# Optimization experiments

Measured on AMD Instinct MI355X. Metric: run time of the kernel, lower is better.

Reference implementation:

```python
import jax, jax.numpy as jnp
import numpy as np

B, N, C, Cn, M = 4, 8192, 128, 64, 32


def _window(x, M):
    # torch F.pad(x, [0,0, M//2, M//2-1]) + unfold(dim=1, size=M, step=1)
    # x: [B, N, Cn] -> [B, N, M, Cn]
    Bx, Nx, Cx = x.shape
    p = M // 2
    xp = jnp.pad(x, ((0, 0), (p, M - 1 - p), (0, 0)))
    idx = jnp.arange(Nx)[:, None] + jnp.arange(M)[None, :]  # [N, M]
    return xp[:, idx, :]  # [B, N, M, Cn]


def setup_inputs() -> dict:
    key = jax.random.key(0)
    ks = jax.random.split(key, 9)
    q = jax.random.normal(ks[0], (B, N, C), dtype=jnp.float32)
    k = jax.random.normal(ks[1], (B, N, C), dtype=jnp.float32)
    v = jax.random.normal(ks[2], (B, N, C), dtype=jnp.float32)
    pe = jax.random.normal(ks[3], (B, N, M, Cn), dtype=jnp.float32)
    # Linear weights stored as [in, out]; scaled like torch default init (~1/sqrt(fan_in)).
    Wq = jax.random.normal(ks[4], (C, Cn), dtype=jnp.float32) / np.sqrt(C)
    Wk = jax.random.normal(ks[5], (C, Cn), dtype=jnp.float32) / np.sqrt(C)
    Wv = jax.random.normal(ks[6], (C, Cn), dtype=jnp.float32) / np.sqrt(C)
    w_sa1 = jax.random.normal(ks[7], (Cn,), dtype=jnp.float32) / np.sqrt(Cn)
    w_sa2 = jax.random.normal(ks[8], (Cn, C), dtype=jnp.float32) / np.sqrt(Cn)
    return {"q": q, "k": k, "v": v, "pe": pe, "Wq": Wq, "Wk": Wk, "Wv": Wv,
            "w_sa1": w_sa1, "w_sa2": w_sa2}


def reference(q, k, v, pe, Wq, Wk, Wv, w_sa1, w_sa2):
    Mw = pe.shape[2]
    qp = q @ Wq  # [B, N, Cn]
    kp = k @ Wk
    vp = v @ Wv
    k_m = _window(kp, Mw)  # [B, N, M, Cn]
    v_m = _window(vp, Mw)  # [B, N, M, Cn]
    # subtraction-based scoring + tiny linear to scalar
    sa = qp[:, :, None, :] - k_m + pe               # [B, N, M, Cn]
    logits = jnp.einsum('bnmc,c->bnm', sa, w_sa1)    # [B, N, M]
    scores = jax.nn.softmax(logits, axis=-1)         # [B, N, M]
    # original: matmul(scores[B,1,N,M], (v_m+pe).permute(0,3,2,1)[B,Cn,M,N]) -> [B,Cn,N,N], sum over last axis.
    # Equivalent: reduce (v_m + pe) over the position axis first, then contract over M.
    S = jnp.sum(v_m + pe, axis=1)                    # [B, M, Cn]
    p_attn = jnp.einsum('bnm,bmc->bnc', scores, S)   # [B, N, Cn]
    out = p_attn @ w_sa2                             # [B, N, C]
    return out  # dropout is identity at eval
```

## Files before the change

kernel.cpp:

```cpp
#include <hip/hip_runtime.h>
#include <math.h>

#define B_ 4
#define N_ 8192
#define C_ 128
#define CN_ 64
#define M_ 32

#define ROR1 0x121
#define ROR2 0x122
#define ROR4 0x124
#define ROR8 0x128

typedef float f4 __attribute__((ext_vector_type(4)));
typedef float f2 __attribute__((ext_vector_type(2)));

__device__ __forceinline__ f4 ld4(const float* p) { return *(const f4*)p; }

template<int CTRL>
__device__ __forceinline__ float dpp_add(float x) {
    int y = __builtin_amdgcn_update_dpp(0, __float_as_int(x), CTRL, 0xF, 0xF, true);
    return x + __int_as_float(y);
}
template<int CTRL>
__device__ __forceinline__ float dpp_max(float x) {
    int y = __builtin_amdgcn_update_dpp(0, __float_as_int(x), CTRL, 0xF, 0xF, true);
    return fmaxf(x, __int_as_float(y));
}
__device__ __forceinline__ float red16_add(float x) {
    return dpp_add<ROR1>(dpp_add<ROR2>(dpp_add<ROR4>(dpp_add<ROR8>(x))));
}
__device__ __forceinline__ float red16_max(float x) {
    return dpp_max<ROR1>(dpp_max<ROR2>(dpp_max<ROR4>(dpp_max<ROR8>(x))));
}

__global__ __launch_bounds__(256) void kA(const float* __restrict__ q,
                                          const float* __restrict__ k,
                                          const float* __restrict__ v,
                                          const float* __restrict__ pe,
                                          const float* __restrict__ Wq,
                                          const float* __restrict__ Wk,
                                          const float* __restrict__ w1,
                                          float* __restrict__ vsum_part,
                                          float* __restrict__ scl_g,
                                          float* __restrict__ pe_part) {
    __shared__ float lpd[4][256];
    __shared__ __align__(16) f4 lps4[4][256];
    __shared__ float pro[352];

    int g = blockIdx.x;
    int t = threadIdx.x;
    int lane = t & 63, wv = t >> 6;

    if (g < 1024) {
        int b = g >> 8;
        int n0 = (g & 255) * 32;
        int grp = lane >> 4, li = lane & 15;
        float* wq1l = pro;
        float* wk1l = pro + 128;
        float* aL   = pro + 256;
        float* kbL  = pro + 288;

        if (t < C_) {
            float s = 0.f;
            for (int c2 = 0; c2 < CN_; ++c2) s += Wq[t * CN_ + c2] * w1[c2];
            wq1l[t] = s;
        } else {
            int c = t - C_;
            float s = 0.f;
            for (int c2 = 0; c2 < CN_; ++c2) s += Wk[c * CN_ + c2] * w1[c2];
            wk1l[c] = s;
        }
        __syncthreads();

        {
            f4 wk0 = *((const f4*)wk1l + li * 2);
            f4 wk1v = *((const f4*)wk1l + li * 2 + 1);
#pragma unroll
            for (int it = 0; it < 4; ++it) {
                int rl = wv * 16 + it * 4 + grp;
                int jrow = n0 - 16 + rl;
                float tk = 0.f;
                if (jrow >= 0 && jrow < N_) {
                    const float* kr = k + ((size_t)b * N_ + jrow) * C_;
                    f4 y0 = ld4(kr + li * 8), y1 = ld4(kr + li * 8 + 4);
                    tk = y0.x * wk0.x + y0.y * wk0.y + y0.z * wk0.z + y0.w * wk0.w
                       + y1.x * wk1v.x + y1.y * wk1v.y + y1.z * wk1v.z + y1.w * wk1v.w;
                }
                tk = red16_add(tk);
                if (li == 0) kbL[rl] = tk;
            }
            f4 wq0 = *((const f4*)wq1l + li * 2);
            f4 wq1v = *((const f4*)wq1l + li * 2 + 1);
#pragma unroll
            for (int it = 0; it < 2; ++it) {
                int rl = wv * 8 + it * 4 + grp;
                const float* qr = q + ((size_t)b * N_ + n0 + rl) * C_;
                f4 x0 = ld4(qr + li * 8), x1 = ld4(qr + li * 8 + 4);
                float ta = x0.x * wq0.x + x0.y * wq0.y + x0.z * wq0.z + x0.w * wq0.w
                         + x1.x * wq1v.x + x1.y * wq1v.y + x1.z * wq1v.z + x1.w * wq1v.w;
                ta = red16_add(ta);
                if (li == 0) aL[rl] = ta;
            }
        }
        __syncthreads();

        f4 w1v = *((const f4*)w1 + li);
        f4 acc[8];
#pragma unroll
        for (int j = 0; j < 8; ++j) acc[j] = (f4){0.f, 0.f, 0.f, 0.f};

        int nbase = n0 + wv * 8;
        const float* pbase = pe + ((size_t)b * N_ + (size_t)nbase) * 2048;
        for (int i = 0; i < 8; ++i) {
            const float* p = pbase + (size_t)i * 2048;
            f4 x[8];
#pragma unroll
            for (int j = 0; j < 8; ++j) x[j] = ld4(p + (j * 64 + lane) * 4);
#pragma unroll
            for (int j = 0; j < 8; ++j) {
                acc[j] += x[j];
                float tv = x[j].x * w1v.x + x[j].y * w1v.y + x[j].z * w1v.z + x[j].w * w1v.w;
                tv = red16_add(tv);
                if (li == 0) lpd[wv][i * 32 + j * 4 + grp] = tv;
            }
        }

        {
            int hw = lane >> 5, m = lane & 31;
            float* sout = scl_g + ((size_t)b * N_ + (size_t)nbase) * M_;
#pragma unroll
            for (int ii = 0; ii < 4; ++ii) {
                int rl = ii * 2 + hw;
                int rb = wv * 8 + rl;
                float pd = lpd[wv][rl * 32 + m];
                float lg = aL[rb] + pd - kbL[rb + m];
                float mx = red16_max(lg);
                mx = fmaxf(mx, __shfl_xor(mx, 16));
                float e = __expf(lg - mx);
                float sm = red16_add(e);
                sm += __shfl_xor(sm, 16);
                sout[ii * 64 + lane] = e / sm;
            }
        }

        f4* ppg = (f4*)(pe_part + (size_t)g * 2048);
#pragma unroll
        for (int r = 0; r < 2; ++r) {
            __syncthreads();
#pragma unroll
            for (int jr = 0; jr < 4; ++jr) lps4[wv][jr * 64 + lane] = acc[r * 4 + jr];
            __syncthreads();
            f4 s = lps4[0][t];
            s += lps4[1][t];
            s += lps4[2][t];
            s += lps4[3][t];
            ppg[r * 256 + t] = s;
        }
    } else {
        int gg = g - 1024;
        int b = gg >> 6;
        int chunk = gg & 63;
        const float* vb = v + ((size_t)b * N_ + (size_t)chunk * 128) * C_;
        int c4 = t & 31, h = t >> 5;
        f4 acc = (f4){0.f, 0.f, 0.f, 0.f};
        for (int r = h; r < 128; r += 8) acc += ld4(vb + (size_t)r * C_ + c4 * 4);
        f4* red = &lps4[0][0];
        red[t] = acc;
        __syncthreads();
        if (t < 32) {
            f4 s = red[t];
#pragma unroll
            for (int i = 1; i < 8; ++i) s += red[i * 32 + t];
            *((f4*)(vsum_part + (size_t)gg * C_) + t) = s;
        }
    }
}

__global__ __launch_bounds__(256) void kR(const float* __restrict__ pe_part,
                                          const float* __restrict__ vsum_part,
                                          float* __restrict__ S_sum,
                                          float* __restrict__ vsum_final) {
    int g = blockIdx.x;
    int t = threadIdx.x;
    if (g < 256) {
        int b = g >> 6, ch = g & 63;
        int pg = t >> 5, fi = t & 31;
        const float* base = pe_part + (size_t)b * 256 * 2048 + ch * 32 + fi;
        float a0 = 0.f, a1 = 0.f, a2 = 0.f, a3 = 0.f;
#pragma unroll
        for (int p = pg; p < 256; p += 32) {
            a0 += base[(size_t)p * 2048];
            a1 += base[(size_t)(p + 8) * 2048];
            a2 += base[(size_t)(p + 16) * 2048];
            a3 += base[(size_t)(p + 24) * 2048];
        }
        __shared__ float red[8][32];
        red[pg][fi] = (a0 + a1) + (a2 + a3);
        __syncthreads();
        if (t < 32) {
            float s = red[0][t];
#pragma unroll
            for (int i = 1; i < 8; ++i) s += red[i][t];
            S_sum[(size_t)b * 2048 + ch * 32 + t] = s;
        }
    } else {
        int b = g - 256;
        if (t < C_) {
            const float* vp = vsum_part + (size_t)b * 64 * C_ + t;
            float a0 = 0.f, a1 = 0.f, a2 = 0.f, a3 = 0.f;
#pragma unroll
            for (int i = 0; i < 64; i += 4) {
                a0 += vp[(i + 0) * C_];
                a1 += vp[(i + 1) * C_];
                a2 += vp[(i + 2) * C_];
                a3 += vp[(i + 3) * C_];
            }
            vsum_final[b * C_ + t] = (a0 + a1) + (a2 + a3);
        }
    }
}

__global__ __launch_bounds__(256) void kB2(const float* __restrict__ v,
                                           const float* __restrict__ Wv,
                                           const float* __restrict__ vsum_final,
                                           const float* __restrict__ S_sum,
                                           const float* __restrict__ w2,
                                           float* __restrict__ SW2) {
    int b = blockIdx.x >> 3, seg = blockIdx.x & 7;
    int t = threadIdx.x;
    __shared__ float vd[4][C_];
    __shared__ float Sl[4][CN_];
#pragma unroll
    for (int mlp = 0; mlp < 2; ++mlp) {
        int ml = (t >> 7) + mlp * 2;
        int c = t & 127;
        int m = seg * 4 + ml;
        float excl = 0.f;
        if (m > 16) {
            for (int r = 0; r < m - 16; ++r) excl += v[((size_t)b * N_ + r) * C_ + c];
        } else if (m < 16) {
            for (int r = N_ - (16 - m); r < N_; ++r) excl += v[((size_t)b * N_ + r) * C_ + c];
        }
        vd[ml][c] = vsum_final[b * C_ + c] - excl;
    }
    __syncthreads();
    {
        int ml = t >> 6, c2 = t & 63;
        float s = 0.f;
        for (int c = 0; c < C_; ++c) s += vd[ml][c] * Wv[c * CN_ + c2];
        s += S_sum[(size_t)b * 2048 + (seg * 4 + ml) * CN_ + c2];
        Sl[ml][c2] = s;
    }
    __syncthreads();
#pragma unroll
    for (int pass = 0; pass < 2; ++pass) {
        int ml = (t >> 7) + pass * 2;
        int cc = t & 127;
        float s = 0.f;
#pragma unroll
        for (int c2 = 0; c2 < CN_; ++c2) s += Sl[ml][c2] * w2[c2 * C_ + cc];
        SW2[((size_t)b * M_ + seg * 4 + ml) * C_ + cc] = s;
    }
}

__global__ __launch_bounds__(256) void kOut2(const float* __restrict__ scl_g,
                                             const float* __restrict__ SW2,
                                             float* __restrict__ out) {
    int g = blockIdx.x;
    int b = g >> 7;
    int n0 = (g & 127) * 64;
    int t = threadIdx.x;
    int lane = t & 63, wv = t >> 6;
    __shared__ float scl[64][M_];

    {
        const f4* src = (const f4*)(scl_g + ((size_t)b * N_ + (size_t)n0) * M_);
        f4* dst = (f4*)&scl[0][0];
        dst[t] = src[t];
        dst[256 + t] = src[256 + t];
    }
    f2 sw2[M_];
    {
        const f2* sw2g = (const f2*)(SW2 + (size_t)b * M_ * C_);
#pragma unroll
        for (int mm = 0; mm < M_; ++mm) sw2[mm] = sw2g[mm * 64 + lane];
    }
    __syncthreads();
    for (int i = 0; i < 16; ++i) {
        int r = wv * 16 + i;
        const f4* sp = (const f4*)(&scl[r][0]);
        float ox = 0.f, oy = 0.f;
#pragma unroll
        for (int j4 = 0; j4 < 8; ++j4) {
            f4 s4 = sp[j4];
            ox += s4.x * sw2[j4 * 4 + 0].x; oy += s4.x * sw2[j4 * 4 + 0].y;
            ox += s4.y * sw2[j4 * 4 + 1].x; oy += s4.y * sw2[j4 * 4 + 1].y;
            ox += s4.z * sw2[j4 * 4 + 2].x; oy += s4.z * sw2[j4 * 4 + 2].y;
            ox += s4.w * sw2[j4 * 4 + 3].x; oy += s4.w * sw2[j4 * 4 + 3].y;
        }
        size_t u = (size_t)b * N_ + (size_t)(n0 + r);
        f2 o; o.x = ox; o.y = oy;
        *((f2*)(out + u * C_) + lane) = o;
    }
}

extern "C" void kernel_launch(void* const* d_in, const int* in_sizes, int n_in,
                              void* d_out, int out_size, void* d_ws, size_t ws_size,
                              hipStream_t stream) {
    const float* q  = (const float*)d_in[0];
    const float* k  = (const float*)d_in[1];
    const float* v  = (const float*)d_in[2];
    const float* pe = (const float*)d_in[3];
    const float* Wq = (const float*)d_in[4];
    const float* Wk = (const float*)d_in[5];
    const float* Wv = (const float*)d_in[6];
    const float* w1 = (const float*)d_in[7];
    const float* w2 = (const float*)d_in[8];
    float* out = (float*)d_out;
    float* ws  = (float*)d_ws;

    float* vsum_part  = ws;
    float* vsum_final = vsum_part + 32768;
    float* scl_g      = vsum_final + 512;
    float* pe_part    = scl_g + 1048576;
    float* S_sum      = pe_part + 2097152;
    float* SW2        = S_sum + 8192;

    kA   <<<1280, 256, 0, stream>>>(q, k, v, pe, Wq, Wk, w1, vsum_part, scl_g, pe_part);
    kR   <<<260, 256, 0, stream>>>(pe_part, vsum_part, S_sum, vsum_final);
    kB2  <<<32, 256, 0, stream>>>(v, Wv, vsum_final, S_sum, w2, SW2);
    kOut2<<<512, 256, 0, stream>>>(scl_g, SW2, out);
}
```

Before: 99.86 us.

## Fold v column-sum blocks into pe blocks and interleave k/q/v loads with pe stream

Removes the separate 256 v-reduction blocks from kA. Each of the 1024 pe blocks now also sums its 32 rows of v, and the k/q projection-dot loads move inside the fully unrolled pe loop so they overlap with the pe streaming. The v partial buffer grows to 256 partials per batch, which kR reduces. Launch bounds now request 4 blocks per SIMD-level occupancy. The risks are higher register pressure from full unrolling and a longer per-block critical path.

```diff
diff --git a/kernel.cpp b/kernel.cpp
--- a/kernel.cpp
+++ b/kernel.cpp
@@ -34,16 +34,20 @@
     return dpp_max<ROR1>(dpp_max<ROR2>(dpp_max<ROR4>(dpp_max<ROR8>(x))));
 }
 
-__global__ __launch_bounds__(256) void kA(const float* __restrict__ q,
-                                          const float* __restrict__ k,
-                                          const float* __restrict__ v,
-                                          const float* __restrict__ pe,
-                                          const float* __restrict__ Wq,
-                                          const float* __restrict__ Wk,
-                                          const float* __restrict__ w1,
-                                          float* __restrict__ vsum_part,
-                                          float* __restrict__ scl_g,
-                                          float* __restrict__ pe_part) {
+__device__ __forceinline__ float dot4(f4 a, f4 b) {
+    return a.x * b.x + a.y * b.y + a.z * b.z + a.w * b.w;
+}
+
+__global__ __launch_bounds__(256, 4) void kA(const float* __restrict__ q,
+                                             const float* __restrict__ k,
+                                             const float* __restrict__ v,
+                                             const float* __restrict__ pe,
+                                             const float* __restrict__ Wq,
+                                             const float* __restrict__ Wk,
+                                             const float* __restrict__ w1,
+                                             float* __restrict__ vsum_part,
+                                             float* __restrict__ scl_g,
+                                             float* __restrict__ pe_part) {
     __shared__ float lpd[4][256];
     __shared__ __align__(16) f4 lps4[4][256];
     __shared__ float pro[352];
@@ -51,129 +55,132 @@
     int g = blockIdx.x;
     int t = threadIdx.x;
     int lane = t & 63, wv = t >> 6;
-
-    if (g < 1024) {
-        int b = g >> 8;
-        int n0 = (g & 255) * 32;
-        int grp = lane >> 4, li = lane & 15;
-        float* wq1l = pro;
-        float* wk1l = pro + 128;
-        float* aL   = pro + 256;
-        float* kbL  = pro + 288;
-
-        if (t < C_) {
-            float s = 0.f;
-            for (int c2 = 0; c2 < CN_; ++c2) s += Wq[t * CN_ + c2] * w1[c2];
-            wq1l[t] = s;
+    int b = g >> 8;
+    int n0 = (g & 255) * 32;
+    int grp = lane >> 4, li = lane & 15;
+    float* wq1l = pro;
+    float* wk1l = pro + 128;
+    float* aL   = pro + 256;
+    float* kbL  = pro + 288;
+
+    if (t < C_) {
+        float s = 0.f;
+        for (int c2 = 0; c2 < CN_; ++c2) s += Wq[t * CN_ + c2] * w1[c2];
+        wq1l[t] = s;
+    } else {
+        int c = t - C_;
+        float s = 0.f;
+        for (int c2 = 0; c2 < CN_; ++c2) s += Wk[c * CN_ + c2] * w1[c2];
+        wk1l[c] = s;
+    }
+    __syncthreads();
+
+    f4 wq0 = *((const f4*)wq1l + li * 2);
+    f4 wq1v = *((const f4*)wq1l + li * 2 + 1);
+    f4 wk0 = *((const f4*)wk1l + li * 2);
+    f4 wk1v = *((const f4*)wk1l + li * 2 + 1);
+    f4 w1v = *((const f4*)w1 + li);
+
+    f4 acc[8];
+#pragma unroll
+    for (int j = 0; j < 8; ++j) acc[j] = (f4){0.f, 0.f, 0.f, 0.f};
+    f4 acc_v = (f4){0.f, 0.f, 0.f, 0.f};
+
+    int nbase = n0 + wv * 8;
+    const float* pbase = pe + ((size_t)b * N_ + (size_t)nbase) * 2048;
+    int hv = lane >> 5, c4 = lane & 31;
+
+#pragma unroll
+    for (int i = 0; i < 8; ++i) {
+        const float* p = pbase + (size_t)i * 2048;
+        f4 x[8];
+#pragma unroll
+        for (int j = 0; j < 8; ++j) x[j] = ld4(p + (j * 64 + lane) * 4);
+
+        f4 s0, s1;
+        bool svalid = false;
+        if (i < 4) {
+            int rl = wv * 16 + i * 4 + grp;
+            int jrow = n0 - 16 + rl;
+            svalid = (jrow >= 0 && jrow < N_);
+            const float* kr = k + ((size_t)b * N_ + (svalid ? jrow : 0)) * C_;
+            s0 = ld4(kr + li * 8);
+            s1 = ld4(kr + li * 8 + 4);
+        } else if (i < 6) {
+            int rl = wv * 8 + (i - 4) * 4 + grp;
+            const float* qr = q + ((size_t)b * N_ + n0 + rl) * C_;
+            s0 = ld4(qr + li * 8);
+            s1 = ld4(qr + li * 8 + 4);
+            svalid = true;
         } else {
-            int c = t - C_;
-            float s = 0.f;
-            for (int c2 = 0; c2 < CN_; ++c2) s += Wk[c * CN_ + c2] * w1[c2];
-            wk1l[c] = s;
-        }
+            int r0 = wv * 8 + hv * 4 + (i - 6) * 2;
+            s0 = ld4(v + ((size_t)b * N_ + n0 + r0) * C_ + c4 * 4);
+            s1 = ld4(v + ((size_t)b * N_ + n0 + r0 + 1) * C_ + c4 * 4);
+        }
+
+#pragma unroll
+        for (int j = 0; j < 8; ++j) {
+            acc[j] += x[j];
+            float tv = dot4(x[j], w1v);
+            tv = red16_add(tv);
+            if (li == 0) lpd[wv][i * 32 + j * 4 + grp] = tv;
+        }
+
+        if (i < 4) {
+            float tk = svalid ? (dot4(s0, wk0) + dot4(s1, wk1v)) : 0.f;
+            tk = red16_add(tk);
+            if (li == 0) kbL[wv * 16 + i * 4 + grp] = tk;
+        } else if (i < 6) {
+            float ta = dot4(s0, wq0) + dot4(s1, wq1v);
+            ta = red16_add(ta);
+            if (li == 0) aL[wv * 8 + (i - 4) * 4 + grp] = ta;
+        } else {
+            acc_v += s0;
+            acc_v += s1;
+        }
+    }
+    __syncthreads();
+
+    {
+        int hw = lane >> 5, m = lane & 31;
+        float* sout = scl_g + ((size_t)b * N_ + (size_t)nbase) * M_;
+#pragma unroll
+        for (int ii = 0; ii < 4; ++ii) {
+            int rl = ii * 2 + hw;
+            int rb = wv * 8 + rl;
+            float pd = lpd[wv][rl * 32 + m];
+            float lg = aL[rb] + pd - kbL[rb + m];
+            float mx = red16_max(lg);
+            mx = fmaxf(mx, __shfl_xor(mx, 16));
+            float e = __expf(lg - mx);
+            float sm = red16_add(e);
+            sm += __shfl_xor(sm, 16);
+            sout[ii * 64 + lane] = e / sm;
+        }
+    }
+
+    f4* ppg = (f4*)(pe_part + (size_t)g * 2048);
+#pragma unroll
+    for (int r = 0; r < 2; ++r) {
         __syncthreads();
-
-        {
-            f4 wk0 = *((const f4*)wk1l + li * 2);
-            f4 wk1v = *((const f4*)wk1l + li * 2 + 1);
-#pragma unroll
-            for (int it = 0; it < 4; ++it) {
-                int rl = wv * 16 + it * 4 + grp;
-                int jrow = n0 - 16 + rl;
-                float tk = 0.f;
-                if (jrow >= 0 && jrow < N_) {
-                    const float* kr = k + ((size_t)b * N_ + jrow) * C_;
-                    f4 y0 = ld4(kr + li * 8), y1 = ld4(kr + li * 8 + 4);
-                    tk = y0.x * wk0.x + y0.y * wk0.y + y0.z * wk0.z + y0.w * wk0.w
-                       + y1.x * wk1v.x + y1.y * wk1v.y + y1.z * wk1v.z + y1.w * wk1v.w;
-                }
-                tk = red16_add(tk);
-                if (li == 0) kbL[rl] = tk;
-            }
-            f4 wq0 = *((const f4*)wq1l + li * 2);
-            f4 wq1v = *((const f4*)wq1l + li * 2 + 1);
-#pragma unroll
-            for (int it = 0; it < 2; ++it) {
-                int rl = wv * 8 + it * 4 + grp;
-                const float* qr = q + ((size_t)b * N_ + n0 + rl) * C_;
-                f4 x0 = ld4(qr + li * 8), x1 = ld4(qr + li * 8 + 4);
-                float ta = x0.x * wq0.x + x0.y * wq0.y + x0.z * wq0.z + x0.w * wq0.w
-                         + x1.x * wq1v.x + x1.y * wq1v.y + x1.z * wq1v.z + x1.w * wq1v.w;
-                ta = red16_add(ta);
-                if (li == 0) aL[rl] = ta;
-            }
-        }
+#pragma unroll
+        for (int jr = 0; jr < 4; ++jr) lps4[wv][jr * 64 + lane] = acc[r * 4 + jr];
         __syncthreads();
-
-        f4 w1v = *((const f4*)w1 + li);
-        f4 acc[8];
-#pragma unroll
-        for (int j = 0; j < 8; ++j) acc[j] = (f4){0.f, 0.f, 0.f, 0.f};
-
-        int nbase = n0 + wv * 8;
-        const float* pbase = pe + ((size_t)b * N_ + (size_t)nbase) * 2048;
-        for (int i = 0; i < 8; ++i) {
-            const float* p = pbase + (size_t)i * 2048;
-            f4 x[8];
-#pragma unroll
-            for (int j = 0; j < 8; ++j) x[j] = ld4(p + (j * 64 + lane) * 4);
-#pragma unroll
-            for (int j = 0; j < 8; ++j) {
-                acc[j] += x[j];
-                float tv = x[j].x * w1v.x + x[j].y * w1v.y + x[j].z * w1v.z + x[j].w * w1v.w;
-                tv = red16_add(tv);
-                if (li == 0) lpd[wv][i * 32 + j * 4 + grp] = tv;
-            }
-        }
-
-        {
-            int hw = lane >> 5, m = lane & 31;
-            float* sout = scl_g + ((size_t)b * N_ + (size_t)nbase) * M_;
-#pragma unroll
-            for (int ii = 0; ii < 4; ++ii) {
-                int rl = ii * 2 + hw;
-                int rb = wv * 8 + rl;
-                float pd = lpd[wv][rl * 32 + m];
-                float lg = aL[rb] + pd - kbL[rb + m];
-                float mx = red16_max(lg);
-                mx = fmaxf(mx, __shfl_xor(mx, 16));
-                float e = __expf(lg - mx);
-                float sm = red16_add(e);
-                sm += __shfl_xor(sm, 16);
-                sout[ii * 64 + lane] = e / sm;
-            }
-        }
-
-        f4* ppg = (f4*)(pe_part + (size_t)g * 2048);
-#pragma unroll
-        for (int r = 0; r < 2; ++r) {
-            __syncthreads();
-#pragma unroll
-            for (int jr = 0; jr < 4; ++jr) lps4[wv][jr * 64 + lane] = acc[r * 4 + jr];
-            __syncthreads();
-            f4 s = lps4[0][t];
-            s += lps4[1][t];
-            s += lps4[2][t];
-            s += lps4[3][t];
-            ppg[r * 256 + t] = s;
-        }
-    } else {
-        int gg = g - 1024;
-        int b = gg >> 6;
-        int chunk = gg & 63;
-        const float* vb = v + ((size_t)b * N_ + (size_t)chunk * 128) * C_;
-        int c4 = t & 31, h = t >> 5;
-        f4 acc = (f4){0.f, 0.f, 0.f, 0.f};
-        for (int r = h; r < 128; r += 8) acc += ld4(vb + (size_t)r * C_ + c4 * 4);
-        f4* red = &lps4[0][0];
-        red[t] = acc;
-        __syncthreads();
-        if (t < 32) {
-            f4 s = red[t];
-#pragma unroll
-            for (int i = 1; i < 8; ++i) s += red[i * 32 + t];
-            *((f4*)(vsum_part + (size_t)gg * C_) + t) = s;
-        }
+        f4 s = lps4[0][t];
+        s += lps4[1][t];
+        s += lps4[2][t];
+        s += lps4[3][t];
+        ppg[r * 256 + t] = s;
+    }
+
+    __syncthreads();
+    lps4[wv][hv * 32 + c4] = acc_v;
+    __syncthreads();
+    if (t < 32) {
+        f4 s = (f4){0.f, 0.f, 0.f, 0.f};
+#pragma unroll
+        for (int w = 0; w < 4; ++w) s += lps4[w][t] + lps4[w][32 + t];
+        *((f4*)(vsum_part + (size_t)g * C_) + t) = s;
     }
 }
 
@@ -207,14 +214,14 @@
     } else {
         int b = g - 256;
         if (t < C_) {
-            const float* vp = vsum_part + (size_t)b * 64 * C_ + t;
+            const float* vp = vsum_part + (size_t)b * 256 * C_ + t;
             float a0 = 0.f, a1 = 0.f, a2 = 0.f, a3 = 0.f;
 #pragma unroll
-            for (int i = 0; i < 64; i += 4) {
-                a0 += vp[(i + 0) * C_];
-                a1 += vp[(i + 1) * C_];
-                a2 += vp[(i + 2) * C_];
-                a3 += vp[(i + 3) * C_];
+            for (int i = 0; i < 256; i += 4) {
+                a0 += vp[(size_t)(i + 0) * C_];
+                a1 += vp[(size_t)(i + 1) * C_];
+                a2 += vp[(size_t)(i + 2) * C_];
+                a3 += vp[(size_t)(i + 3) * C_];
             }
             vsum_final[b * C_ + t] = (a0 + a1) + (a2 + a3);
         }
@@ -321,13 +328,13 @@
     float* ws  = (float*)d_ws;
 
     float* vsum_part  = ws;
-    float* vsum_final = vsum_part + 32768;
+    float* vsum_final = vsum_part + 131072;
     float* scl_g      = vsum_final + 512;
     float* pe_part    = scl_g + 1048576;
     float* S_sum      = pe_part + 2097152;
     float* SW2        = S_sum + 8192;
 
-    kA   <<<1280, 256, 0, stream>>>(q, k, v, pe, Wq, Wk, w1, vsum_part, scl_g, pe_part);
+    kA   <<<1024, 256, 0, stream>>>(q, k, v, pe, Wq, Wk, w1, vsum_part, scl_g, pe_part);
     kR   <<<260, 256, 0, stream>>>(pe_part, vsum_part, S_sum, vsum_final);
     kB2  <<<32, 256, 0, stream>>>(v, Wv, vsum_final, S_sum, w2, SW2);
     kOut2<<<512, 256, 0, stream>>>(scl_g, SW2, out);
```

Result: slower. 185.1 us (+85.4%).
